# Optimization experiments

Measured on AMD Instinct MI355X. Metric: run time of the kernel, lower is better.

Reference implementation:

```python
import jax, jax.numpy as jnp
import numpy as np

IN_FEATURES = 1024
FEATURES = 1024
GRID_SIZE = 5
SPLINE_ORDER = 3
GRID_MIN, GRID_MAX = -2.0, 2.0
EPS = 1e-7


def setup_inputs() -> dict:
    key = jax.random.key(0)
    k_x, k_w, k_ss, k_bs = jax.random.split(key, 4)
    x = jax.random.normal(k_x, (4096, IN_FEATURES), dtype=jnp.float32)
    # Extended knot sequence: grid_size + 2*spline_order + 1 knots
    h = (GRID_MAX - GRID_MIN) / GRID_SIZE
    grid = GRID_MIN + h * jnp.arange(-SPLINE_ORDER, GRID_SIZE + SPLINE_ORDER + 1,
                                     dtype=jnp.float32)  # (12,)
    K = GRID_SIZE + SPLINE_ORDER  # number of B-spline basis functions = 8
    # glorot_uniform over (I, O, K)
    limit = float(np.sqrt(6.0 / (IN_FEATURES + FEATURES)))
    spline_weight = jax.random.uniform(k_w, (IN_FEATURES, FEATURES, K),
                                       minval=-limit, maxval=limit, dtype=jnp.float32)
    spline_scaler = jax.random.uniform(k_ss, (IN_FEATURES, FEATURES),
                                       minval=-limit, maxval=limit, dtype=jnp.float32)
    base_scaler = jax.random.uniform(k_bs, (IN_FEATURES, FEATURES),
                                     minval=-limit, maxval=limit, dtype=jnp.float32)
    return {"x": x, "grid": grid, "spline_weight": spline_weight,
            "spline_scaler": spline_scaler, "base_scaler": base_scaler}


def _bspline_bases(x, grid):
    # x: (B, I); grid: (G+2S+1,) -> bases: (B, I, G+S)
    xe = x[..., None]
    # order-0 indicator bases on each knot interval
    bases = ((xe >= grid[:-1]) & (xe < grid[1:])).astype(x.dtype)
    for p in range(1, SPLINE_ORDER + 1):  # Cox-de Boor recursion
        left = (xe - grid[:-(p + 1)]) / (grid[p:-1] - grid[:-(p + 1)] + EPS)
        right = (grid[p + 1:] - xe) / (grid[p + 1:] - grid[1:-p] + EPS)
        bases = left * bases[..., :-1] + right * bases[..., 1:]
    return bases


def reference(x, grid, spline_weight, spline_scaler, base_scaler):
    # Base path: b(x) = swish(x) = x * sigmoid(x), summed over inputs with base_scaler
    base_out = jnp.einsum('bi,io->bo', x * jax.nn.sigmoid(x), base_scaler)
    # Spline path: per-connection spline with per-connection scaling
    bases = _bspline_bases(x, grid)                       # (B, I, K)
    scaled_w = spline_weight * spline_scaler[..., None]   # (I, O, K)
    spline_out = jnp.einsum('bik,iok->bo', bases, scaled_w)
    return base_out + spline_out
```

## Files before the change

### kernel.cpp

```cpp
#include <hip/hip_runtime.h>
#include <hip/hip_bf16.h>
#include <cstdint>
#include <cstddef>

#define I_F   1024
#define O_F   1024
#define BATCH 4096
#define KDIM  9216
#define EPSC  1e-7f

typedef __bf16 bf16;
typedef __bf16 bf16x4 __attribute__((ext_vector_type(4)));
typedef __bf16 bf16x8 __attribute__((ext_vector_type(8)));
typedef float  f32x4  __attribute__((ext_vector_type(4)));

__global__ __launch_bounds__(256) void prep_kernel(const float* __restrict__ x,
                                                   const float* __restrict__ grid,
                                                   const float* __restrict__ w,
                                                   const float* __restrict__ ss,
                                                   const float* __restrict__ bs,
                                                   bf16* __restrict__ A,
                                                   bf16* __restrict__ Wt) {
    if (blockIdx.x < 512) {
        int g = blockIdx.x * 256 + threadIdx.x;
        int i  = g & 1023;
        int o0 = (g >> 10) << 3;
        size_t io0 = (size_t)i * 1024 + o0;
        f32x4 ssv0 = *(const f32x4*)(ss + io0);
        f32x4 ssv1 = *(const f32x4*)(ss + io0 + 4);
        f32x4 bsv0 = *(const f32x4*)(bs + io0);
        f32x4 bsv1 = *(const f32x4*)(bs + io0 + 4);
#pragma unroll
        for (int oo = 0; oo < 8; ++oo) {
            int o = o0 + oo;
            float scale = (oo < 4) ? ssv0[oo & 3] : ssv1[oo & 3];
            float base  = (oo < 4) ? bsv0[oo & 3] : bsv1[oo & 3];
            const float* wp = w + (io0 + oo) * 8;
            f32x4 w0 = *(const f32x4*)(wp);
            f32x4 w1 = *(const f32x4*)(wp + 4);

            bf16* outp = Wt + (size_t)o * KDIM + i;
            outp[0] = (bf16)base;
#pragma unroll
            for (int k = 0; k < 4; ++k) outp[(size_t)(k + 1) * 1024] = (bf16)(w0[k] * scale);
#pragma unroll
            for (int k = 0; k < 4; ++k) outp[(size_t)(k + 5) * 1024] = (bf16)(w1[k] * scale);
        }
    } else {
        int t  = (blockIdx.x - 512) * 256 + threadIdx.x;
        int b  = t >> 8;
        int i0 = (t & 255) << 2;
        f32x4 xv4 = *(const f32x4*)(x + (size_t)b * I_F + i0);

        float g[12];
#pragma unroll
        for (int j = 0; j < 12; ++j) g[j] = grid[j];
        float r1[11], r2[10], r3[9];
#pragma unroll
        for (int j = 0; j < 11; ++j) r1[j] = __builtin_amdgcn_rcpf(g[j + 1] - g[j] + EPSC);
#pragma unroll
        for (int j = 0; j < 10; ++j) r2[j] = __builtin_amdgcn_rcpf(g[j + 2] - g[j] + EPSC);
#pragma unroll
        for (int j = 0; j < 9;  ++j) r3[j] = __builtin_amdgcn_rcpf(g[j + 3] - g[j] + EPSC);

        float sw[4];
        float bs8[4][8];
#pragma unroll
        for (int e = 0; e < 4; ++e) {
            float xv = xv4[e];
            float bas[11];
#pragma unroll
            for (int j = 0; j < 11; ++j)
                bas[j] = (xv >= g[j] && xv < g[j + 1]) ? 1.0f : 0.0f;
#pragma unroll
            for (int j = 0; j < 10; ++j)
                bas[j] = (xv - g[j]) * r1[j] * bas[j] + (g[j + 2] - xv) * r1[j + 1] * bas[j + 1];
#pragma unroll
            for (int j = 0; j < 9; ++j)
                bas[j] = (xv - g[j]) * r2[j] * bas[j] + (g[j + 3] - xv) * r2[j + 1] * bas[j + 1];
#pragma unroll
            for (int j = 0; j < 8; ++j)
                bas[j] = (xv - g[j]) * r3[j] * bas[j] + (g[j + 4] - xv) * r3[j + 1] * bas[j + 1];
#pragma unroll
            for (int k = 0; k < 8; ++k) bs8[e][k] = bas[k];
            float sig = 1.0f / (1.0f + __expf(-xv));
            sw[e] = xv * sig;
        }

        bf16* outp = A + (size_t)b * KDIM + i0;
        *(bf16x4*)(outp) = (bf16x4){(bf16)sw[0], (bf16)sw[1], (bf16)sw[2], (bf16)sw[3]};
#pragma unroll
        for (int k = 0; k < 8; ++k)
            *(bf16x4*)(outp + (size_t)(k + 1) * 1024) =
                (bf16x4){(bf16)bs8[0][k], (bf16)bs8[1][k], (bf16)bs8[2][k], (bf16)bs8[3][k]};
    }
}

__device__ __forceinline__ void load_lds16(const bf16* g, bf16* l) {
    __builtin_amdgcn_global_load_lds(
        (__attribute__((address_space(1))) void*)g,
        (__attribute__((address_space(3))) void*)l, 16, 0, 0);
}

__global__ __launch_bounds__(512, 1) void gemm_kernel(const bf16* __restrict__ A,
                                                      const bf16* __restrict__ Wt,
                                                      bf16* __restrict__ parts,
                                                      int split, int ktiles) {
    __shared__ __align__(16) bf16 SA[2][16384];
    __shared__ __align__(16) bf16 SB[2][16384];

    const int t    = threadIdx.x;
    const int lane = t & 63;
    const int w    = t >> 6;

    const int nwg8 = gridDim.x >> 3;
    const int L    = (blockIdx.x & 7) * nwg8 + (blockIdx.x >> 3);
    const int nper = split << 4;
    const int tn   = L / nper;
    const int rem  = L - tn * nper;
    const int s    = rem >> 4;
    const int tm   = rem & 15;

    const int row0 = tm << 8;
    const int col0 = tn << 8;
    const size_t k0 = (size_t)s * ktiles * 64;

    const int sr8 = lane >> 3;
    const int lc  = (lane & 7) ^ sr8;
    const bf16* gA0 = A  + (size_t)(row0 + w * 32 + sr8) * KDIM + k0 + lc * 8;
    const bf16* gB0 = Wt + (size_t)(col0 + w * 32 + sr8) * KDIM + k0 + lc * 8;

    const int wm  = w >> 2;
    const int wn  = w & 3;
    const int r15 = lane & 15;
    const int g4  = lane >> 4;
    const int rx7 = r15 & 7;

    f32x4 acc[8][4];
#pragma unroll
    for (int mt = 0; mt < 8; ++mt)
#pragma unroll
        for (int nt = 0; nt < 4; ++nt) acc[mt][nt] = (f32x4){0.f, 0.f, 0.f, 0.f};

    auto stage = [&](int j) {
        const int sl = j & 1;
        const bf16* pa = gA0 + (size_t)j * 64;
        const bf16* pb = gB0 + (size_t)j * 64;
#pragma unroll
        for (int q = 0; q < 4; ++q)
            load_lds16(pa + (size_t)(q * 8) * KDIM, &SA[sl][(w * 32 + q * 8) * 64]);
#pragma unroll
        for (int q = 0; q < 4; ++q)
            load_lds16(pb + (size_t)(q * 8) * KDIM, &SB[sl][(w * 32 + q * 8) * 64]);
    };

    auto frag_load = [&](int sl, int ks, bf16x8 (&af)[8], bf16x8 (&bv)[4]) {
        const int cp = (((ks * 4 + g4) ^ rx7) << 3);
        af[0] = *(const bf16x8*)&SA[sl][(wm * 128 + 0 * 16 + r15) * 64 + cp];
#pragma unroll
        for (int nt = 0; nt < 4; ++nt)
            bv[nt] = *(const bf16x8*)&SB[sl][(wn * 64 + nt * 16 + r15) * 64 + cp];
#pragma unroll
        for (int mt = 1; mt < 8; ++mt)
            af[mt] = *(const bf16x8*)&SA[sl][(wm * 128 + mt * 16 + r15) * 64 + cp];
    };

    auto do_mfma = [&](bf16x8 (&af)[8], bf16x8 (&bv)[4]) {
        __builtin_amdgcn_s_setprio(1);
#pragma unroll
        for (int mt = 0; mt < 8; ++mt)
#pragma unroll
            for (int nt = 0; nt < 4; ++nt)
                acc[mt][nt] = __builtin_amdgcn_mfma_f32_16x16x32_bf16(
                    af[mt], bv[nt], acc[mt][nt], 0, 0, 0);
        __builtin_amdgcn_s_setprio(0);
    };

    stage(0);

    for (int j = 0; j < ktiles; ++j) {
        asm volatile("s_waitcnt vmcnt(0)" ::: "memory");
        __builtin_amdgcn_s_barrier();
        asm volatile("" ::: "memory");
        bf16x8 af0[8], bv0[4], af1[8], bv1[4];
        frag_load(j & 1, 0, af0, bv0);
        if (j + 1 < ktiles) stage(j + 1);
        do_mfma(af0, bv0);
        frag_load(j & 1, 1, af1, bv1);
        do_mfma(af1, bv1);
    }

    bf16* cp2 = parts + (size_t)s * BATCH * O_F
              + (size_t)(row0 + wm * 128) * O_F + col0 + wn * 64 + r15;
#pragma unroll
    for (int mt = 0; mt < 8; ++mt)
#pragma unroll
        for (int nt = 0; nt < 4; ++nt)
#pragma unroll
            for (int r = 0; r < 4; ++r)
                cp2[(size_t)(mt * 16 + g4 * 4 + r) * O_F + nt * 16] = (bf16)acc[mt][nt][r];
}

__global__ __launch_bounds__(256) void add_kernel(float* __restrict__ out,
                                                  const bf16* __restrict__ parts,
                                                  int np) {
    int t = blockIdx.x * 256 + threadIdx.x;
    f32x4 a = {0.f, 0.f, 0.f, 0.f};
    for (int p = 0; p < np; ++p) {
        bf16x4 b = *((const bf16x4*)(parts + (size_t)p * BATCH * O_F) + t);
#pragma unroll
        for (int e = 0; e < 4; ++e) a[e] += (float)b[e];
    }
    *((f32x4*)out + t) = a;
}

extern "C" void kernel_launch(void* const* d_in, const int* in_sizes, int n_in,
                              void* d_out, int out_size, void* d_ws, size_t ws_size,
                              hipStream_t stream) {
    const float* x    = (const float*)d_in[0];
    const float* grid = (const float*)d_in[1];
    const float* w    = (const float*)d_in[2];
    const float* ss   = (const float*)d_in[3];
    const float* bs   = (const float*)d_in[4];
    float* out = (float*)d_out;

    const size_t nA = (size_t)BATCH * KDIM * 2;
    const size_t nW = (size_t)O_F   * KDIM * 2;
    const size_t nP = (size_t)BATCH * O_F  * 2;

    bf16* A  = (bf16*)d_ws;
    bf16* Wt = (bf16*)((char*)d_ws + nA);
    bf16* parts = (bf16*)((char*)d_ws + nA + nW);

    prep_kernel<<<4608, 256, 0, stream>>>(x, grid, w, ss, bs, A, Wt);

    int split = (ws_size >= nA + nW + 4 * nP) ? 4
              : (ws_size >= nA + nW + 2 * nP) ? 2 : 1;
    gemm_kernel<<<64 * split, 512, 0, stream>>>(A, Wt, parts, split, 144 / split);
    add_kernel<<<(BATCH * O_F / 4) / 256, 256, 0, stream>>>(out, parts, split);
}
```

Before: 109.6 us.

## Add BK=32 GEMM variant with two blocks per CU and split-K of eight

Adds a GEMM kernel with a 32-wide K tile that halves LDS use to 64 KB, so two workgroups can share a CU (launch bounds 512,2). It also raises split-K to 8, launching 512 workgroups instead of 256 to fill the 256 CUs, when the workspace is large enough. The original 64-wide kernel is kept as a fallback for smaller workspaces. In exchange it doubles the partial-sum writes and the add-kernel reads, and the accumulators must fit in half the register file per wave.

```diff
diff --git a/kernel.cpp b/kernel.cpp
--- a/kernel.cpp
+++ b/kernel.cpp
@@ -102,12 +102,12 @@
         (__attribute__((address_space(3))) void*)l, 16, 0, 0);
 }
 
-__global__ __launch_bounds__(512, 1) void gemm_kernel(const bf16* __restrict__ A,
-                                                      const bf16* __restrict__ Wt,
-                                                      bf16* __restrict__ parts,
-                                                      int split, int ktiles) {
-    __shared__ __align__(16) bf16 SA[2][16384];
-    __shared__ __align__(16) bf16 SB[2][16384];
+__global__ __launch_bounds__(512, 2) void gemm32_kernel(const bf16* __restrict__ A,
+                                                        const bf16* __restrict__ Wt,
+                                                        bf16* __restrict__ parts,
+                                                        int split, int ktiles) {
+    __shared__ __align__(16) bf16 SA[2][8192];
+    __shared__ __align__(16) bf16 SB[2][8192];
 
     const int t    = threadIdx.x;
     const int lane = t & 63;
@@ -123,6 +123,100 @@
 
     const int row0 = tm << 8;
     const int col0 = tn << 8;
+    const size_t k0 = (size_t)s * ktiles * 32;
+
+    const int sr = lane >> 2;
+    const int lc = (lane & 3) ^ ((lane >> 3) & 3);
+    const bf16* gA0 = A  + (size_t)(row0 + w * 16 + sr) * KDIM + k0 + lc * 8;
+    const bf16* gB0 = Wt + (size_t)(col0 + w * 16 + sr) * KDIM + k0 + lc * 8;
+
+    const int wm  = w >> 2;
+    const int wn  = w & 3;
+    const int r15 = lane & 15;
+    const int g4  = lane >> 4;
+    const int swb = (r15 >> 1) & 3;
+    const int cp  = ((g4 ^ swb) << 3);
+
+    f32x4 acc[8][4];
+#pragma unroll
+    for (int mt = 0; mt < 8; ++mt)
+#pragma unroll
+        for (int nt = 0; nt < 4; ++nt) acc[mt][nt] = (f32x4){0.f, 0.f, 0.f, 0.f};
+
+    auto stage = [&](int j) {
+        const int sl = j & 1;
+        const bf16* pa = gA0 + (size_t)j * 32;
+        const bf16* pb = gB0 + (size_t)j * 32;
+        load_lds16(pa,                      &SA[sl][w * 512]);
+        load_lds16(pa + (size_t)128 * KDIM, &SA[sl][4096 + w * 512]);
+        load_lds16(pb,                      &SB[sl][w * 512]);
+        load_lds16(pb + (size_t)128 * KDIM, &SB[sl][4096 + w * 512]);
+    };
+
+    auto frag_load = [&](int sl, bf16x8 (&af)[8], bf16x8 (&bv)[4]) {
+        af[0] = *(const bf16x8*)&SA[sl][(wm * 128 + 0 * 16 + r15) * 32 + cp];
+#pragma unroll
+        for (int nt = 0; nt < 4; ++nt)
+            bv[nt] = *(const bf16x8*)&SB[sl][(wn * 64 + nt * 16 + r15) * 32 + cp];
+#pragma unroll
+        for (int mt = 1; mt < 8; ++mt)
+            af[mt] = *(const bf16x8*)&SA[sl][(wm * 128 + mt * 16 + r15) * 32 + cp];
+    };
+
+    auto do_mfma = [&](bf16x8 (&af)[8], bf16x8 (&bv)[4]) {
+        __builtin_amdgcn_s_setprio(1);
+#pragma unroll
+        for (int mt = 0; mt < 8; ++mt)
+#pragma unroll
+            for (int nt = 0; nt < 4; ++nt)
+                acc[mt][nt] = __builtin_amdgcn_mfma_f32_16x16x32_bf16(
+                    af[mt], bv[nt], acc[mt][nt], 0, 0, 0);
+        __builtin_amdgcn_s_setprio(0);
+    };
+
+    stage(0);
+    for (int j = 0; j < ktiles; ++j) {
+        asm volatile("s_waitcnt vmcnt(0)" ::: "memory");
+        __builtin_amdgcn_s_barrier();
+        asm volatile("" ::: "memory");
+        bf16x8 af[8], bv[4];
+        frag_load(j & 1, af, bv);
+        if (j + 1 < ktiles) stage(j + 1);
+        do_mfma(af, bv);
+    }
+
+    bf16* cp2 = parts + (size_t)s * BATCH * O_F
+              + (size_t)(row0 + wm * 128) * O_F + col0 + wn * 64 + r15;
+#pragma unroll
+    for (int mt = 0; mt < 8; ++mt)
+#pragma unroll
+        for (int nt = 0; nt < 4; ++nt)
+#pragma unroll
+            for (int r = 0; r < 4; ++r)
+                cp2[(size_t)(mt * 16 + g4 * 4 + r) * O_F + nt * 16] = (bf16)acc[mt][nt][r];
+}
+
+__global__ __launch_bounds__(512, 1) void gemm64_kernel(const bf16* __restrict__ A,
+                                                        const bf16* __restrict__ Wt,
+                                                        bf16* __restrict__ parts,
+                                                        int split, int ktiles) {
+    __shared__ __align__(16) bf16 SA[2][16384];
+    __shared__ __align__(16) bf16 SB[2][16384];
+
+    const int t    = threadIdx.x;
+    const int lane = t & 63;
+    const int w    = t >> 6;
+
+    const int nwg8 = gridDim.x >> 3;
+    const int L    = (blockIdx.x & 7) * nwg8 + (blockIdx.x >> 3);
+    const int nper = split << 4;
+    const int tn   = L / nper;
+    const int rem  = L - tn * nper;
+    const int s    = rem >> 4;
+    const int tm   = rem & 15;
+
+    const int row0 = tm << 8;
+    const int col0 = tn << 8;
     const size_t k0 = (size_t)s * ktiles * 64;
 
     const int sr8 = lane >> 3;
@@ -177,7 +271,6 @@
     };
 
     stage(0);
-
     for (int j = 0; j < ktiles; ++j) {
         asm volatile("s_waitcnt vmcnt(0)" ::: "memory");
         __builtin_amdgcn_s_barrier();
@@ -234,8 +327,14 @@
 
     prep_kernel<<<4608, 256, 0, stream>>>(x, grid, w, ss, bs, A, Wt);
 
-    int split = (ws_size >= nA + nW + 4 * nP) ? 4
-              : (ws_size >= nA + nW + 2 * nP) ? 2 : 1;
-    gemm_kernel<<<64 * split, 512, 0, stream>>>(A, Wt, parts, split, 144 / split);
-    add_kernel<<<(BATCH * O_F / 4) / 256, 256, 0, stream>>>(out, parts, split);
-}
+    if (ws_size >= nA + nW + 8 * nP) {
+        gemm32_kernel<<<64 * 8, 512, 0, stream>>>(A, Wt, parts, 8, 288 / 8);
+        add_kernel<<<(BATCH * O_F / 4) / 256, 256, 0, stream>>>(out, parts, 8);
+    } else if (ws_size >= nA + nW + 4 * nP) {
+        gemm64_kernel<<<64 * 4, 512, 0, stream>>>(A, Wt, parts, 4, 144 / 4);
+        add_kernel<<<(BATCH * O_F / 4) / 256, 256, 0, stream>>>(out, parts, 4);
+    } else {
+        gemm64_kernel<<<64 * 2, 512, 0, stream>>>(A, Wt, parts, 2, 144 / 2);
+        add_kernel<<<(BATCH * O_F / 4) / 256, 256, 0, stream>>>(out, parts, 2);
+    }
+}
```

Result: slower. 126.4 us (+15.4%).

## Split GEMM k-tile into four barrier-synchronised chunks interleaving LDS reads and staging

Applied to the files above, without the earlier changes.

Restructures the main GEMM loop so each k-tile is processed in four chunks of two M-subtiles. Each chunk loads its A fragments for both k-steps, while the B fragments for the whole tile are loaded once. The global-to-LDS staging of A and B for the next tile is split across the first two chunks. Workgroup barriers around each MFMA chunk keep waves in lockstep, in the style of ping-pong scheduling. The aim is to spread memory traffic and overlap it with MFMA work, at the cost of eight extra barriers per tile.

```diff
diff --git a/kernel.cpp b/kernel.cpp
--- a/kernel.cpp
+++ b/kernel.cpp
@@ -142,52 +142,97 @@
 #pragma unroll
         for (int nt = 0; nt < 4; ++nt) acc[mt][nt] = (f32x4){0.f, 0.f, 0.f, 0.f};
 
-    auto stage = [&](int j) {
+    auto stage_A = [&](int j) {
         const int sl = j & 1;
         const bf16* pa = gA0 + (size_t)j * 64;
-        const bf16* pb = gB0 + (size_t)j * 64;
 #pragma unroll
         for (int q = 0; q < 4; ++q)
             load_lds16(pa + (size_t)(q * 8) * KDIM, &SA[sl][(w * 32 + q * 8) * 64]);
+    };
+    auto stage_B = [&](int j) {
+        const int sl = j & 1;
+        const bf16* pb = gB0 + (size_t)j * 64;
 #pragma unroll
         for (int q = 0; q < 4; ++q)
             load_lds16(pb + (size_t)(q * 8) * KDIM, &SB[sl][(w * 32 + q * 8) * 64]);
     };
 
-    auto frag_load = [&](int sl, int ks, bf16x8 (&af)[8], bf16x8 (&bv)[4]) {
-        const int cp = (((ks * 4 + g4) ^ rx7) << 3);
-        af[0] = *(const bf16x8*)&SA[sl][(wm * 128 + 0 * 16 + r15) * 64 + cp];
+    auto frag_a2 = [&](int sl, int q, bf16x8 (&af)[2][2]) {
+#pragma unroll
+        for (int m2 = 0; m2 < 2; ++m2)
+#pragma unroll
+            for (int ks = 0; ks < 2; ++ks)
+                af[m2][ks] = *(const bf16x8*)&SA[sl][
+                    (wm * 128 + (2 * q + m2) * 16 + r15) * 64
+                    + (((ks * 4 + g4) ^ rx7) << 3)];
+    };
+    auto frag_ball = [&](int sl, bf16x8 (&bv)[4][2]) {
 #pragma unroll
         for (int nt = 0; nt < 4; ++nt)
-            bv[nt] = *(const bf16x8*)&SB[sl][(wn * 64 + nt * 16 + r15) * 64 + cp];
-#pragma unroll
-        for (int mt = 1; mt < 8; ++mt)
-            af[mt] = *(const bf16x8*)&SA[sl][(wm * 128 + mt * 16 + r15) * 64 + cp];
-    };
-
-    auto do_mfma = [&](bf16x8 (&af)[8], bf16x8 (&bv)[4]) {
+#pragma unroll
+            for (int ks = 0; ks < 2; ++ks)
+                bv[nt][ks] = *(const bf16x8*)&SB[sl][
+                    (wn * 64 + nt * 16 + r15) * 64
+                    + (((ks * 4 + g4) ^ rx7) << 3)];
+    };
+
+    auto chunk = [&](int q, bf16x8 (&af)[2][2], bf16x8 (&bv)[4][2]) {
         __builtin_amdgcn_s_setprio(1);
 #pragma unroll
-        for (int mt = 0; mt < 8; ++mt)
-#pragma unroll
-            for (int nt = 0; nt < 4; ++nt)
-                acc[mt][nt] = __builtin_amdgcn_mfma_f32_16x16x32_bf16(
-                    af[mt], bv[nt], acc[mt][nt], 0, 0, 0);
+        for (int ks = 0; ks < 2; ++ks)
+#pragma unroll
+            for (int m2 = 0; m2 < 2; ++m2)
+#pragma unroll
+                for (int nt = 0; nt < 4; ++nt)
+                    acc[2 * q + m2][nt] = __builtin_amdgcn_mfma_f32_16x16x32_bf16(
+                        af[m2][ks], bv[nt][ks], acc[2 * q + m2][nt], 0, 0, 0);
         __builtin_amdgcn_s_setprio(0);
     };
 
-    stage(0);
+    stage_A(0); stage_B(0);
 
     for (int j = 0; j < ktiles; ++j) {
         asm volatile("s_waitcnt vmcnt(0)" ::: "memory");
         __builtin_amdgcn_s_barrier();
         asm volatile("" ::: "memory");
-        bf16x8 af0[8], bv0[4], af1[8], bv1[4];
-        frag_load(j & 1, 0, af0, bv0);
-        if (j + 1 < ktiles) stage(j + 1);
-        do_mfma(af0, bv0);
-        frag_load(j & 1, 1, af1, bv1);
-        do_mfma(af1, bv1);
+        const int sl = j & 1;
+        bf16x8 bv[4][2];
+
+        {
+            bf16x8 af[2][2];
+            frag_ball(sl, bv);
+            frag_a2(sl, 0, af);
+            if (j + 1 < ktiles) stage_A(j + 1);
+            __builtin_amdgcn_s_barrier();
+            chunk(0, af, bv);
+            __builtin_amdgcn_s_barrier();
+            asm volatile("" ::: "memory");
+        }
+        {
+            bf16x8 af[2][2];
+            frag_a2(sl, 1, af);
+            if (j + 1 < ktiles) stage_B(j + 1);
+            __builtin_amdgcn_s_barrier();
+            chunk(1, af, bv);
+            __builtin_amdgcn_s_barrier();
+            asm volatile("" ::: "memory");
+        }
+        {
+            bf16x8 af[2][2];
+            frag_a2(sl, 2, af);
+            __builtin_amdgcn_s_barrier();
+            chunk(2, af, bv);
+            __builtin_amdgcn_s_barrier();
+            asm volatile("" ::: "memory");
+        }
+        {
+            bf16x8 af[2][2];
+            frag_a2(sl, 3, af);
+            __builtin_amdgcn_s_barrier();
+            chunk(3, af, bv);
+            __builtin_amdgcn_s_barrier();
+            asm volatile("" ::: "memory");
+        }
     }
 
     bf16* cp2 = parts + (size_t)s * BATCH * O_F
```

Measured after the change: 126.4 us. 15.4% more time.
